# Kernel tuning notes

Measured on AMD Instinct MI355X. Metric: run time of the kernel, lower is better.

## Reference

```python
import math
import jax, jax.numpy as jnp
import numpy as np

NUM_HEADS = 12
NUM_LANDMARKS = 32

def iterative_inv(mat, n_iter=6):
    # mat: [B, H, m, m] row-stochastic kernel; Newton-Schulz pseudo-inverse
    m = mat.shape[-1]
    I = jnp.eye(m, dtype=mat.dtype)
    K = mat
    # 'else' branch: per-(B,H) normalization by max column sum
    denom = jnp.max(jnp.sum(K, axis=-2), axis=-1)[..., None, None]
    V = jnp.swapaxes(K, -1, -2) / denom
    for _ in range(n_iter):
        KV = jnp.matmul(K, V)
        V = jnp.matmul(0.25 * V, 13.0 * I - jnp.matmul(KV, 15.0 * I - jnp.matmul(KV, 7.0 * I - KV)))
    return V

def setup_inputs() -> dict:
    key = jax.random.key(0)
    k1, k2, k3 = jax.random.split(key, 3)
    B, N, C = 8, 2048, 768
    x = jax.random.normal(k1, (B, N, C), dtype=jnp.float32)
    w_qkv = jax.random.normal(k2, (C, 3 * C), dtype=jnp.float32) * (1.0 / math.sqrt(C))
    w_proj = jax.random.normal(k3, (C, C), dtype=jnp.float32) * (1.0 / math.sqrt(C))
    b_proj = jnp.zeros((C,), dtype=jnp.float32)
    return {"x": x, "w_qkv": w_qkv, "w_proj": w_proj, "b_proj": b_proj}

def reference(x, w_qkv, w_proj, b_proj):
    B, N, C = x.shape
    H = NUM_HEADS
    d = C // H
    m = NUM_LANDMARKS
    qkv = (x @ w_qkv).reshape(B, N, 3, H, d).transpose(2, 0, 3, 1, 4)  # [3,B,H,N,d]
    Q, K, V = qkv[0], qkv[1], qkv[2]
    scale = 1.0 / math.sqrt(math.sqrt(d))
    Q = Q * scale
    K = K * scale
    # landmark pooling: mean over contiguous chunks of size N//m
    Q_l = Q.reshape(B, H, m, N // m, d).mean(axis=-2)  # [B,H,m,d]
    K_l = K.reshape(B, H, m, N // m, d).mean(axis=-2)
    kernel_1 = jax.nn.softmax(jnp.einsum('bhnd,bhmd->bhnm', Q, K_l), axis=-1)   # [B,H,N,m]
    kernel_2 = jax.nn.softmax(jnp.einsum('bhmd,bhkd->bhmk', Q_l, K_l), axis=-1) # [B,H,m,m]
    kernel_3 = jax.nn.softmax(jnp.einsum('bhmd,bhnd->bhmn', Q_l, K), axis=-1)   # [B,H,m,N]
    X = jnp.matmul(jnp.matmul(kernel_1, iterative_inv(kernel_2)), jnp.matmul(kernel_3, V))  # [B,H,N,d]
    X = X.transpose(0, 2, 1, 3).reshape(B, N, C)
    return X @ w_proj + b_proj
```

## Files before the change

### kernel.cpp

```cpp
#include <hip/hip_runtime.h>
#include <hip/hip_bf16.h>

typedef __hip_bfloat16 bf16;
typedef __attribute__((ext_vector_type(8))) __bf16 bf16x8;
typedef __attribute__((ext_vector_type(4))) float f32x4;

#define NB 8
#define SEQ 2048
#define CH 768
#define NH 12
#define HD 64
#define NL 32
#define BHT (NB*NH)
#define TOK (NB*SEQ)
#define QK_SCALE 0.35355339059327379f

#define BAR() __builtin_amdgcn_s_barrier()
#define WLGKM0() __asm__ __volatile__("s_waitcnt lgkmcnt(0)" ::: "memory")
#define WVM(n) __asm__ __volatile__("s_waitcnt vmcnt(" #n ")" ::: "memory")

__device__ __forceinline__ void async_ld16(const bf16* g, bf16* l) {
    unsigned loff = (unsigned)__builtin_amdgcn_readfirstlane((int)(unsigned)(uintptr_t)l);
    __builtin_amdgcn_global_load_lds(
        (const __attribute__((address_space(1))) unsigned*)(uintptr_t)g,
        (__attribute__((address_space(3))) unsigned*)(uintptr_t)loff, 16, 0, 0);
}

__global__ void convert_x(const float* __restrict__ x, bf16* __restrict__ xb) {
    size_t i = ((size_t)blockIdx.x * 256 + threadIdx.x) * 8;
    float4 a = *reinterpret_cast<const float4*>(x + i);
    float4 b = *reinterpret_cast<const float4*>(x + i + 4);
    alignas(16) bf16 tmp[8];
    tmp[0] = __float2bfloat16(a.x); tmp[1] = __float2bfloat16(a.y);
    tmp[2] = __float2bfloat16(a.z); tmp[3] = __float2bfloat16(a.w);
    tmp[4] = __float2bfloat16(b.x); tmp[5] = __float2bfloat16(b.y);
    tmp[6] = __float2bfloat16(b.z); tmp[7] = __float2bfloat16(b.w);
    *reinterpret_cast<uint4*>(xb + i) = *reinterpret_cast<const uint4*>(tmp);
}

__global__ void transpose_f32(const float* __restrict__ in, bf16* __restrict__ outp,
                              int Hrows, int Wcols) {
    __shared__ float tile[32][33];
    int bx = blockIdx.x * 32, by = blockIdx.y * 32;
    int tx = threadIdx.x, ty = threadIdx.y;
    for (int i = 0; i < 32; i += 8)
        tile[ty + i][tx] = in[(size_t)(by + ty + i) * Wcols + bx + tx];
    __syncthreads();
    for (int i = 0; i < 32; i += 8)
        outp[(size_t)(bx + ty + i) * Hrows + by + tx] = __float2bfloat16(tile[tx][ty + i]);
}

template <int EPI>
__global__ __launch_bounds__(512, 2) void gemm_bt(
    const bf16* __restrict__ A, const bf16* __restrict__ Bt,
    int Nout, int Kdim,
    bf16* __restrict__ q, bf16* __restrict__ k, bf16* __restrict__ vt,
    float* __restrict__ Ql, float* __restrict__ Kl,
    float* __restrict__ outp, const float* __restrict__ bias_f) {
    __shared__ __align__(16) bf16 As[2][256 * 64];
    __shared__ __align__(16) bf16 Bs[2][192 * 64];
    const int t = threadIdx.x;
    const int wave = t >> 6, lane = t & 63;
    const int quad = lane >> 4, l15 = lane & 15;
    const int wr = wave >> 2, wc = wave & 3;

    int p = blockIdx.y * gridDim.x + blockIdx.x;
    int xcd = p & 7, j = p >> 3;
    int gx = gridDim.x;
    int bn = j % gx;
    int bm = (j / gx) * 8 + xcd;
    const int bm0 = bm * 256;
    const int bn0 = bn * 192;

    const int T = Kdim >> 6;

    const int srow = t >> 3;
    const int scol = (((t & 7) ^ (srow & 7)) << 3);
    const bf16* Abase = A + (size_t)(bm0 + srow) * Kdim + scol;
    const bf16* Bbase = Bt + (size_t)(bn0 + srow) * Kdim + scol;

    auto stA = [&](int kt, int c) {
        async_ld16(Abase + (size_t)(c * 64) * Kdim + kt * 64,
                   &As[kt & 1][c * 4096 + t * 8]);
    };
    auto stB = [&](int kt, int c) {
        async_ld16(Bbase + (size_t)(c * 64) * Kdim + kt * 64,
                   &Bs[kt & 1][c * 4096 + t * 8]);
    };

    const int swk[2] = { (quad ^ (l15 & 7)) << 3, ((4 + quad) ^ (l15 & 7)) << 3 };
    const bf16* arow = &As[0][(wr * 128 + l15) * 64];
    const bf16* brow = &Bs[0][(wc * 48 + l15) * 64];

    f32x4 acc[8][3];
    const f32x4 zero4 = {0.f, 0.f, 0.f, 0.f};
    #pragma unroll
    for (int i = 0; i < 8; i++)
        #pragma unroll
        for (int jj = 0; jj < 3; jj++) acc[i][jj] = zero4;

    stA(0, 0); stA(0, 2); stB(0, 0); stB(0, 1); stB(0, 2); stA(0, 1); stA(0, 3);
    WVM(2);
    BAR();

    bf16x8 a[4][2], b[3][2];
    #pragma unroll 2
    for (int kt = 0; kt < T; kt++) {
        const int cur = kt & 1;
        const bool nxt = (kt + 1 < T);
        const bf16* ab = arow + cur * 16384;
        const bf16* bb = brow + cur * 12288;

        #pragma unroll
        for (int mi = 0; mi < 4; mi++)
            #pragma unroll
            for (int kk = 0; kk < 2; kk++)
                a[mi][kk] = *reinterpret_cast<const bf16x8*>(ab + mi * 1024 + swk[kk]);
        #pragma unroll
        for (int ni = 0; ni < 2; ni++)
            #pragma unroll
            for (int kk = 0; kk < 2; kk++)
                b[ni][kk] = *reinterpret_cast<const bf16x8*>(bb + ni * 1024 + swk[kk]);
        if (nxt) { stA(kt + 1, 0); stA(kt + 1, 2); }
        BAR(); WLGKM0();
        __builtin_amdgcn_s_setprio(1);
        #pragma unroll
        for (int mi = 0; mi < 4; mi++)
            #pragma unroll
            for (int ni = 0; ni < 2; ni++)
                #pragma unroll
                for (int kk = 0; kk < 2; kk++)
                    acc[mi][ni] = __builtin_amdgcn_mfma_f32_16x16x32_bf16(a[mi][kk], b[ni][kk], acc[mi][ni], 0, 0, 0);
        __builtin_amdgcn_s_setprio(0);
        BAR();

        #pragma unroll
        for (int kk = 0; kk < 2; kk++)
            b[2][kk] = *reinterpret_cast<const bf16x8*>(bb + 2 * 1024 + swk[kk]);
        if (nxt) { stB(kt + 1, 0); stB(kt + 1, 1); }
        BAR(); WLGKM0();
        __builtin_amdgcn_s_setprio(1);
        #pragma unroll
        for (int mi = 0; mi < 4; mi++)
            #pragma unroll
            for (int kk = 0; kk < 2; kk++)
                acc[mi][2] = __builtin_amdgcn_mfma_f32_16x16x32_bf16(a[mi][kk], b[2][kk], acc[mi][2], 0, 0, 0);
        __builtin_amdgcn_s_setprio(0);
        if (nxt) { WVM(4); } else { WVM(0); }
        BAR();

        #pragma unroll
        for (int mi = 0; mi < 4; mi++)
            #pragma unroll
            for (int kk = 0; kk < 2; kk++)
                a[mi][kk] = *reinterpret_cast<const bf16x8*>(ab + (mi + 4) * 1024 + swk[kk]);
        if (nxt) { stB(kt + 1, 2); stA(kt + 1, 1); }
        BAR(); WLGKM0();
        __builtin_amdgcn_s_setprio(1);
        #pragma unroll
        for (int mi = 0; mi < 4; mi++)
            #pragma unroll
            for (int ni = 0; ni < 2; ni++)
                #pragma unroll
                for (int kk = 0; kk < 2; kk++)
                    acc[mi + 4][ni] = __builtin_amdgcn_mfma_f32_16x16x32_bf16(a[mi][kk], b[ni][kk], acc[mi + 4][ni], 0, 0, 0);
        __builtin_amdgcn_s_setprio(0);
        BAR();

        if (nxt) { stA(kt + 1, 3); }
        BAR();
        __builtin_amdgcn_s_setprio(1);
        #pragma unroll
        for (int mi = 0; mi < 4; mi++)
            #pragma unroll
            for (int kk = 0; kk < 2; kk++)
                acc[mi + 4][2] = __builtin_amdgcn_mfma_f32_16x16x32_bf16(a[mi][kk], b[2][kk], acc[mi + 4][2], 0, 0, 0);
        __builtin_amdgcn_s_setprio(0);
        WVM(2);
        BAR();
    }

    if (EPI == 0) {
        const int which = bn0 / CH;
        const int rem0 = bn0 - which * CH + wc * 48;
        const int b = bm0 >> 11;
        const int nnb = (bm0 & 2047) + wr * 128;
        if (which < 2) {
            bf16* dstqk = (which == 0) ? q : k;
            float* dstl = (which == 0) ? Ql : Kl;
            const int la0 = nnb >> 6;
            #pragma unroll
            for (int hf = 0; hf < 2; hf++) {
                #pragma unroll
                for (int ni = 0; ni < 3; ni++) {
                    int rem = rem0 + ni * 16;
                    int h = rem >> 6;
                    int dd = (rem & 63) + l15;
                    int bh = b * NH + h;
                    float colsum = 0.f;
                    #pragma unroll
                    for (int m2 = 0; m2 < 4; m2++) {
                        int mi = hf * 4 + m2;
                        int nn0 = nnb + mi * 16 + quad * 4;
                        #pragma unroll
                        for (int r = 0; r < 4; r++) {
                            float val = acc[mi][ni][r];
                            colsum += val;
                            dstqk[((size_t)bh * SEQ + nn0 + r) * HD + dd] = __float2bfloat16(val * QK_SCALE);
                        }
                    }
                    colsum += __shfl_xor(colsum, 16);
                    colsum += __shfl_xor(colsum, 32);
                    if (quad == 0)
                        dstl[((size_t)bh * NL + la0 + hf) * HD + dd] = colsum * (QK_SCALE / 64.f);
                }
            }
        } else {
            #pragma unroll
            for (int ni = 0; ni < 3; ni++) {
                int rem = rem0 + ni * 16;
                int h = rem >> 6;
                int dd = (rem & 63) + l15;
                int bh = b * NH + h;
                #pragma unroll
                for (int mi = 0; mi < 8; mi++) {
                    int nn0 = nnb + mi * 16 + quad * 4;
                    alignas(8) bf16 four[4];
                    #pragma unroll
                    for (int r = 0; r < 4; r++) four[r] = __float2bfloat16(acc[mi][ni][r]);
                    *reinterpret_cast<uint2*>(&vt[((size_t)bh * HD + dd) * SEQ + nn0]) =
                        *reinterpret_cast<const uint2*>(four);
                }
            }
        }
    } else {
        #pragma unroll
        for (int ni = 0; ni < 3; ni++) {
            int col = bn0 + wc * 48 + ni * 16 + l15;
            float bb = bias_f[col];
            #pragma unroll
            for (int mi = 0; mi < 8; mi++)
                #pragma unroll
                for (int r = 0; r < 4; r++) {
                    int row = bm0 + wr * 128 + mi * 16 + quad * 4 + r;
                    outp[(size_t)row * Nout + col] = acc[mi][ni][r] + bb;
                }
        }
    }
}

__device__ inline void mm32(float* Cm, const float* Am, const float* Bm, int t) {
    for (int e = t; e < 1024; e += 256) {
        int i = e >> 5, jj = e & 31;
        float s = 0.f;
        #pragma unroll
        for (int kk = 0; kk < 32; kk++) s += Am[i * 32 + kk] * Bm[kk * 32 + jj];
        Cm[e] = s;
    }
}

__global__ __launch_bounds__(256) void k3_pv(const float* __restrict__ Ql,
                                             const float* __restrict__ Klm,
                                             const bf16* __restrict__ Kb,
                                             const bf16* __restrict__ Vt,
                                             float* __restrict__ Opart,
                                             float* __restrict__ Spart,
                                             float* __restrict__ Vinv) {
    __shared__ __align__(16) char smem[69632];
    const int bh = blockIdx.x;
    const int t = threadIdx.x;

    if (blockIdx.y == 0) {
        float* K2 = (float*)smem;
        float* Vv = K2 + 1024;
        float* KV = K2 + 2048;
        float* Ta = K2 + 3072;
        float* Tb = K2 + 4096;
        float* red = K2 + 5120;
        const float* ql = Ql + (size_t)bh * NL * HD;
        const float* kl = Klm + (size_t)bh * NL * HD;

        for (int e = t; e < 1024; e += 256) {
            int i = e >> 5, jj = e & 31;
            float s = 0.f;
            #pragma unroll 8
            for (int d = 0; d < 64; d++) s += ql[i * 64 + d] * kl[jj * 64 + d];
            K2[e] = s;
        }
        __syncthreads();
        if (t < 32) {
            float mx = -1e30f;
            for (int jj = 0; jj < 32; jj++) mx = fmaxf(mx, K2[t * 32 + jj]);
            float sm = 0.f;
            for (int jj = 0; jj < 32; jj++) { float e = __expf(K2[t * 32 + jj] - mx); K2[t * 32 + jj] = e; sm += e; }
            float inv = 1.f / sm;
            for (int jj = 0; jj < 32; jj++) K2[t * 32 + jj] *= inv;
        }
        __syncthreads();
        if (t < 32) {
            float cs = 0.f;
            for (int i = 0; i < 32; i++) cs += K2[i * 32 + t];
            red[t] = cs;
        }
        __syncthreads();
        if (t == 0) {
            float mx = red[0];
            for (int jj = 1; jj < 32; jj++) mx = fmaxf(mx, red[jj]);
            red[32] = mx;
        }
        __syncthreads();
        float invden = 1.f / red[32];
        for (int e = t; e < 1024; e += 256) {
            int i = e >> 5, jj = e & 31;
            Vv[e] = K2[jj * 32 + i] * invden;
        }
        __syncthreads();
        for (int it = 0; it < 6; it++) {
            mm32(KV, K2, Vv, t);
            __syncthreads();
            for (int e = t; e < 1024; e += 256) { int i = e >> 5, jj = e & 31; Ta[e] = ((i == jj) ? 7.f : 0.f) - KV[e]; }
            __syncthreads();
            mm32(Tb, KV, Ta, t);
            __syncthreads();
            for (int e = t; e < 1024; e += 256) { int i = e >> 5, jj = e & 31; Tb[e] = ((i == jj) ? 15.f : 0.f) - Tb[e]; }
            __syncthreads();
            mm32(Ta, KV, Tb, t);
            __syncthreads();
            for (int e = t; e < 1024; e += 256) { int i = e >> 5, jj = e & 31; Ta[e] = ((i == jj) ? 13.f : 0.f) - Ta[e]; }
            __syncthreads();
            mm32(Tb, Vv, Ta, t);
            __syncthreads();
            for (int e = t; e < 1024; e += 256) Vv[e] = 0.25f * Tb[e];
            __syncthreads();
        }
        for (int e = t; e < 1024; e += 256)
            Vinv[(size_t)bh * 1024 + e] = Vv[e];
        return;
    }

    bf16* Pw0 = (bf16*)smem;
    float* Ored0 = (float*)(smem + 34816);
    float* Sred = (float*)(smem + 34816 + 33280);
    const int cc = blockIdx.y - 1;
    const int n0 = cc * 512;
    const int w = t >> 6, lane = t & 63;
    const int quad = lane >> 4, l15 = lane & 15;

    const bf16* Kbh = Kb + (size_t)bh * SEQ * HD;
    const bf16* Vtb = Vt + (size_t)bh * HD * SEQ;

    bf16x8 af[2][2];
    #pragma unroll
    for (int mt = 0; mt < 2; mt++)
        #pragma unroll
        for (int kh = 0; kh < 2; kh++) {
            const float* src = Ql + (size_t)bh * NL * HD + (mt * 16 + l15) * 64 + kh * 32 + quad * 8;
            alignas(16) bf16 tmp[8];
            #pragma unroll
            for (int jj = 0; jj < 8; jj++) tmp[jj] = __float2bfloat16(src[jj]);
            af[mt][kh] = *reinterpret_cast<const bf16x8*>(tmp);
        }

    const f32x4 zero4 = {0.f, 0.f, 0.f, 0.f};
    f32x4 oacc[2][4];
    #pragma unroll
    for (int mt = 0; mt < 2; mt++)
        #pragma unroll
        for (int nd = 0; nd < 4; nd++) oacc[mt][nd] = zero4;
    float rs[2][4];
    #pragma unroll
    for (int mt = 0; mt < 2; mt++)
        #pragma unroll
        for (int r = 0; r < 4; r++) rs[mt][r] = 0.f;

    bf16* Pme = Pw0 + w * (32 * 136);

    #pragma unroll
    for (int h = 0; h < 2; h++) {
        f32x4 sacc[2][4];
        #pragma unroll
        for (int mt = 0; mt < 2; mt++)
            #pragma unroll
            for (int nt = 0; nt < 4; nt++) sacc[mt][nt] = zero4;
        #pragma unroll
        for (int nt = 0; nt < 4; nt++) {
            int n = n0 + w * 128 + h * 64 + nt * 16 + l15;
            bf16x8 kf0 = *reinterpret_cast<const bf16x8*>(&Kbh[(size_t)n * HD + quad * 8]);
            bf16x8 kf1 = *reinterpret_cast<const bf16x8*>(&Kbh[(size_t)n * HD + 32 + quad * 8]);
            #pragma unroll
            for (int mt = 0; mt < 2; mt++) {
                sacc[mt][nt] = __builtin_amdgcn_mfma_f32_16x16x32_bf16(af[mt][0], kf0, sacc[mt][nt], 0, 0, 0);
                sacc[mt][nt] = __builtin_amdgcn_mfma_f32_16x16x32_bf16(af[mt][1], kf1, sacc[mt][nt], 0, 0, 0);
            }
        }
        #pragma unroll
        for (int mt = 0; mt < 2; mt++)
            #pragma unroll
            for (int nt = 0; nt < 4; nt++)
                #pragma unroll
                for (int r = 0; r < 4; r++) {
                    float pv = __expf(sacc[mt][nt][r]);
                    rs[mt][r] += pv;
                    int row = mt * 16 + quad * 4 + r;
                    Pme[row * 136 + h * 64 + nt * 16 + l15] = __float2bfloat16(pv);
                }
    }
    __asm__ __volatile__("s_waitcnt lgkmcnt(0)" ::: "memory");

    #pragma unroll
    for (int kt = 0; kt < 4; kt++) {
        bf16x8 pa[2];
        pa[0] = *reinterpret_cast<const bf16x8*>(&Pme[l15 * 136 + kt * 32 + quad * 8]);
        pa[1] = *reinterpret_cast<const bf16x8*>(&Pme[(16 + l15) * 136 + kt * 32 + quad * 8]);
        int kbase = n0 + w * 128 + kt * 32 + quad * 8;
        #pragma unroll
        for (int nd = 0; nd < 4; nd++) {
            bf16x8 bv = *reinterpret_cast<const bf16x8*>(&Vtb[(size_t)(nd * 16 + l15) * SEQ + kbase]);
            oacc[0][nd] = __builtin_amdgcn_mfma_f32_16x16x32_bf16(pa[0], bv, oacc[0][nd], 0, 0, 0);
            oacc[1][nd] = __builtin_amdgcn_mfma_f32_16x16x32_bf16(pa[1], bv, oacc[1][nd], 0, 0, 0);
        }
    }

    #pragma unroll
    for (int mt = 0; mt < 2; mt++)
        #pragma unroll
        for (int r = 0; r < 4; r++) {
            float v = rs[mt][r];
            #pragma unroll
            for (int o = 1; o < 16; o <<= 1) v += __shfl_xor(v, o);
            rs[mt][r] = v;
        }
    if (l15 == 0)
        #pragma unroll
        for (int mt = 0; mt < 2; mt++)
            #pragma unroll
            for (int r = 0; r < 4; r++)
                Sred[w * 32 + mt * 16 + quad * 4 + r] = rs[mt][r];
    #pragma unroll
    for (int mt = 0; mt < 2; mt++)
        #pragma unroll
        for (int nd = 0; nd < 4; nd++)
            #pragma unroll
            for (int r = 0; r < 4; r++)
                Ored0[w * (32 * 65) + (mt * 16 + quad * 4 + r) * 65 + nd * 16 + l15] = oacc[mt][nd][r];
    __syncthreads();

    float* Op = Opart + ((size_t)bh * 4 + cc) * (NL * HD);
    for (int e = t; e < 2048; e += 256) {
        int m = e >> 6, dd = e & 63;
        Op[e] = Ored0[0 * (32 * 65) + m * 65 + dd] + Ored0[1 * (32 * 65) + m * 65 + dd] +
                Ored0[2 * (32 * 65) + m * 65 + dd] + Ored0[3 * (32 * 65) + m * 65 + dd];
    }
    if (t < 32)
        Spart[((size_t)bh * 4 + cc) * NL + t] = Sred[t] + Sred[32 + t] + Sred[64 + t] + Sred[96 + t];
}

__global__ __launch_bounds__(256) void combine_w2(const float* __restrict__ Opart,
                                                  const float* __restrict__ Spart,
                                                  const float* __restrict__ Vinv,
                                                  float* __restrict__ W2) {
    __shared__ float K3[2048];
    __shared__ float Vv[1024];
    __shared__ float stot[32];
    const int bh = blockIdx.x;
    const int t = threadIdx.x;

    if (t < 32) {
        const float* sp = Spart + (size_t)bh * 4 * NL;
        stot[t] = sp[t] + sp[32 + t] + sp[64 + t] + sp[96 + t];
    }
    {
        const float* op = Opart + (size_t)bh * 4 * (NL * HD);
        for (int e = t; e < 2048; e += 256)
            K3[e] = op[e] + op[2048 + e] + op[4096 + e] + op[6144 + e];
    }
    for (int e = t; e < 1024; e += 256)
        Vv[e] = Vinv[(size_t)bh * 1024 + e];
    __syncthreads();
    for (int e = t; e < 2048; e += 256) K3[e] *= (1.f / stot[e >> 6]);
    __syncthreads();
    for (int e = t; e < 2048; e += 256) {
        int i = e >> 6, dd = e & 63;
        float s = 0.f;
        #pragma unroll
        for (int kk = 0; kk < 32; kk++) s += Vv[i * 32 + kk] * K3[kk * 64 + dd];
        W2[(size_t)bh * NL * HD + e] = s;
    }
}

__global__ __launch_bounds__(256) void rows_fused(const bf16* __restrict__ Qb,
                                                  const float* __restrict__ Kl,
                                                  const float* __restrict__ W2,
                                                  bf16* __restrict__ Xp) {
    __shared__ __align__(16) bf16 Klb[32 * 64];
    __shared__ __align__(16) bf16 W2t[64 * 32];
    __shared__ __align__(16) bf16 Pw[4][32 * 40];
    const int bh = blockIdx.x, tile = blockIdx.y;
    const int t = threadIdx.x, w = t >> 6, lane = t & 63;
    const int quad = lane >> 4, l15 = lane & 15;

    {
        const float* ksrc = Kl + (size_t)bh * NL * HD;
        const float* wsrc = W2 + (size_t)bh * NL * HD;
        int e0 = t * 8;
        #pragma unroll
        for (int jj = 0; jj < 8; jj++) {
            int e = e0 + jj;
            Klb[e] = __float2bfloat16(ksrc[e]);
            int kk = e >> 6, dd = e & 63;
            W2t[dd * 32 + kk] = __float2bfloat16(wsrc[e]);
        }
    }
    __syncthreads();

    const int b = bh / NH, h = bh - b * NH;
    const int row0 = tile * 128 + w * 32;
    const bf16* qbase = Qb + ((size_t)bh * SEQ + row0) * HD;

    const f32x4 zero4 = {0.f, 0.f, 0.f, 0.f};
    f32x4 sacc[2][2];
    #pragma unroll
    for (int mt = 0; mt < 2; mt++)
        #pragma unroll
        for (int nt = 0; nt < 2; nt++) sacc[mt][nt] = zero4;
    #pragma unroll
    for (int kh = 0; kh < 2; kh++) {
        bf16x8 bk0 = *reinterpret_cast<const bf16x8*>(&Klb[(l15) * 64 + kh * 32 + quad * 8]);
        bf16x8 bk1 = *reinterpret_cast<const bf16x8*>(&Klb[(16 + l15) * 64 + kh * 32 + quad * 8]);
        #pragma unroll
        for (int mt = 0; mt < 2; mt++) {
            bf16x8 aq = *reinterpret_cast<const bf16x8*>(&qbase[(size_t)(mt * 16 + l15) * HD + kh * 32 + quad * 8]);
            sacc[mt][0] = __builtin_amdgcn_mfma_f32_16x16x32_bf16(aq, bk0, sacc[mt][0], 0, 0, 0);
            sacc[mt][1] = __builtin_amdgcn_mfma_f32_16x16x32_bf16(aq, bk1, sacc[mt][1], 0, 0, 0);
        }
    }

    float invs[2][4];
    bf16* Pme = &Pw[w][0];
    #pragma unroll
    for (int mt = 0; mt < 2; mt++)
        #pragma unroll
        for (int r = 0; r < 4; r++) {
            float v0 = __expf(sacc[mt][0][r]);
            float v1 = __expf(sacc[mt][1][r]);
            int row = mt * 16 + quad * 4 + r;
            Pme[row * 40 + l15] = __float2bfloat16(v0);
            Pme[row * 40 + 16 + l15] = __float2bfloat16(v1);
            float v = v0 + v1;
            #pragma unroll
            for (int o = 1; o < 16; o <<= 1) v += __shfl_xor(v, o);
            invs[mt][r] = 1.f / v;
        }
    __asm__ __volatile__("s_waitcnt lgkmcnt(0)" ::: "memory");

    f32x4 oacc[2][4];
    #pragma unroll
    for (int mt = 0; mt < 2; mt++)
        #pragma unroll
        for (int nd = 0; nd < 4; nd++) oacc[mt][nd] = zero4;
    bf16x8 pa[2];
    pa[0] = *reinterpret_cast<const bf16x8*>(&Pme[l15 * 40 + quad * 8]);
    pa[1] = *reinterpret_cast<const bf16x8*>(&Pme[(16 + l15) * 40 + quad * 8]);
    #pragma unroll
    for (int nd = 0; nd < 4; nd++) {
        bf16x8 bw = *reinterpret_cast<const bf16x8*>(&W2t[(nd * 16 + l15) * 32 + quad * 8]);
        oacc[0][nd] = __builtin_amdgcn_mfma_f32_16x16x32_bf16(pa[0], bw, oacc[0][nd], 0, 0, 0);
        oacc[1][nd] = __builtin_amdgcn_mfma_f32_16x16x32_bf16(pa[1], bw, oacc[1][nd], 0, 0, 0);
    }

    #pragma unroll
    for (int mt = 0; mt < 2; mt++)
        #pragma unroll
        for (int nd = 0; nd < 4; nd++)
            #pragma unroll
            for (int r = 0; r < 4; r++) {
                int row = row0 + mt * 16 + quad * 4 + r;
                Xp[((size_t)(b * SEQ + row)) * CH + h * 64 + nd * 16 + l15] =
                    __float2bfloat16(oacc[mt][nd][r] * invs[mt][r]);
            }
}

extern "C" void kernel_launch(void* const* d_in, const int* in_sizes, int n_in,
                              void* d_out, int out_size, void* d_ws, size_t ws_size,
                              hipStream_t stream) {
    const float* x      = (const float*)d_in[0];
    const float* w_qkv  = (const float*)d_in[1];
    const float* w_proj = (const float*)d_in[2];
    const float* b_proj = (const float*)d_in[3];
    float* out = (float*)d_out;

    char* ws = (char*)d_ws;
    size_t off = 0;
    auto alloc = [&](size_t bytes) -> void* {
        void* p = ws + off;
        off += (bytes + 255) & ~(size_t)255;
        return p;
    };
    bf16* wqkvT  = (bf16*)alloc((size_t)3 * CH * CH * 2);
    bf16* wprojT = (bf16*)alloc((size_t)CH * CH * 2);
    bf16* Qb     = (bf16*)alloc((size_t)BHT * SEQ * HD * 2);
    bf16* Kb     = (bf16*)alloc((size_t)BHT * SEQ * HD * 2);
    bf16* Vt     = (bf16*)alloc((size_t)BHT * SEQ * HD * 2);
    float* Ql    = (float*)alloc((size_t)BHT * NL * HD * 4);
    float* Kl    = (float*)alloc((size_t)BHT * NL * HD * 4);
    float* Opart = (float*)alloc((size_t)BHT * 4 * NL * HD * 4);
    float* Spart = (float*)alloc((size_t)BHT * 4 * NL * 4);
    float* Vinv  = (float*)alloc((size_t)BHT * NL * NL * 4);
    float* W2    = (float*)alloc((size_t)BHT * NL * HD * 4);
    bf16* Xp     = (bf16*)alloc((size_t)TOK * CH * 2);
    if (ws_size < off) return;
    bf16* xb = Xp;

    convert_x<<<TOK * CH / 2048, 256, 0, stream>>>(x, xb);
    transpose_f32<<<dim3((3 * CH) / 32, CH / 32), dim3(32, 8), 0, stream>>>(w_qkv, wqkvT, CH, 3 * CH);
    transpose_f32<<<dim3(CH / 32, CH / 32), dim3(32, 8), 0, stream>>>(w_proj, wprojT, CH, CH);

    gemm_bt<0><<<dim3((3 * CH) / 192, TOK / 256), 512, 0, stream>>>(
        xb, wqkvT, 3 * CH, CH, Qb, Kb, Vt, Ql, Kl, nullptr, nullptr);

    k3_pv<<<dim3(BHT, 5), 256, 0, stream>>>(Ql, Kl, Kb, Vt, Opart, Spart, Vinv);
    combine_w2<<<BHT, 256, 0, stream>>>(Opart, Spart, Vinv, W2);
    rows_fused<<<dim3(BHT, SEQ / 128), 256, 0, stream>>>(Qb, Kl, W2, Xp);

    gemm_bt<1><<<dim3(CH / 192, TOK / 256), 512, 0, stream>>>(
        Xp, wprojT, CH, CH, nullptr, nullptr, nullptr, nullptr, nullptr, out, b_proj);
}
```

Before: 277.2 us.

## Fuse prep kernels, merge landmark inverse with PV pass, remap GEMM tiles

Merges the x conversion and both weight transposes into one prep launch. Fuses the Newton-Schulz inverse, the kernel_3·V pass and the W2 combine into a single kernel per (batch, head), removing the Opart/Spart/Vinv round trips and two launches. The price is that each block now runs the inverse and then loops serially over all 2048 tokens, so parallelism drops from 480 blocks to 96. Also changes the GEMM tile mapping so each XCD gets a contiguous range of row tiles.

```diff
diff --git a/kernel.cpp b/kernel.cpp
--- a/kernel.cpp
+++ b/kernel.cpp
@@ -26,23 +26,38 @@
         (__attribute__((address_space(3))) unsigned*)(uintptr_t)loff, 16, 0, 0);
 }
 
-__global__ void convert_x(const float* __restrict__ x, bf16* __restrict__ xb) {
-    size_t i = ((size_t)blockIdx.x * 256 + threadIdx.x) * 8;
-    float4 a = *reinterpret_cast<const float4*>(x + i);
-    float4 b = *reinterpret_cast<const float4*>(x + i + 4);
-    alignas(16) bf16 tmp[8];
-    tmp[0] = __float2bfloat16(a.x); tmp[1] = __float2bfloat16(a.y);
-    tmp[2] = __float2bfloat16(a.z); tmp[3] = __float2bfloat16(a.w);
-    tmp[4] = __float2bfloat16(b.x); tmp[5] = __float2bfloat16(b.y);
-    tmp[6] = __float2bfloat16(b.z); tmp[7] = __float2bfloat16(b.w);
-    *reinterpret_cast<uint4*>(xb + i) = *reinterpret_cast<const uint4*>(tmp);
-}
-
-__global__ void transpose_f32(const float* __restrict__ in, bf16* __restrict__ outp,
-                              int Hrows, int Wcols) {
+#define PREP_G0 (TOK*CH/2048)
+#define PREP_G1 ((3*CH/32)*(CH/32))
+#define PREP_G2 ((CH/32)*(CH/32))
+__global__ __launch_bounds__(256) void prep(const float* __restrict__ x, bf16* __restrict__ xb,
+                                            const float* __restrict__ w_qkv, bf16* __restrict__ wqkvT,
+                                            const float* __restrict__ w_proj, bf16* __restrict__ wprojT) {
     __shared__ float tile[32][33];
-    int bx = blockIdx.x * 32, by = blockIdx.y * 32;
-    int tx = threadIdx.x, ty = threadIdx.y;
+    const int bid = blockIdx.x;
+    const int t = threadIdx.x;
+    if (bid < PREP_G0) {
+        size_t i = ((size_t)bid * 256 + t) * 8;
+        float4 a = *reinterpret_cast<const float4*>(x + i);
+        float4 b = *reinterpret_cast<const float4*>(x + i + 4);
+        alignas(16) bf16 tmp[8];
+        tmp[0] = __float2bfloat16(a.x); tmp[1] = __float2bfloat16(a.y);
+        tmp[2] = __float2bfloat16(a.z); tmp[3] = __float2bfloat16(a.w);
+        tmp[4] = __float2bfloat16(b.x); tmp[5] = __float2bfloat16(b.y);
+        tmp[6] = __float2bfloat16(b.z); tmp[7] = __float2bfloat16(b.w);
+        *reinterpret_cast<uint4*>(xb + i) = *reinterpret_cast<const uint4*>(tmp);
+        return;
+    }
+    const float* in; bf16* outp; int Hrows, Wcols, bx, by;
+    if (bid < PREP_G0 + PREP_G1) {
+        int tb = bid - PREP_G0;
+        in = w_qkv; outp = wqkvT; Hrows = CH; Wcols = 3 * CH;
+        bx = (tb % (3 * CH / 32)) * 32; by = (tb / (3 * CH / 32)) * 32;
+    } else {
+        int tb = bid - PREP_G0 - PREP_G1;
+        in = w_proj; outp = wprojT; Hrows = CH; Wcols = CH;
+        bx = (tb % (CH / 32)) * 32; by = (tb / (CH / 32)) * 32;
+    }
+    int tx = t & 31, ty = t >> 5;
     for (int i = 0; i < 32; i += 8)
         tile[ty + i][tx] = in[(size_t)(by + ty + i) * Wcols + bx + tx];
     __syncthreads();
@@ -65,10 +80,10 @@
     const int wr = wave >> 2, wc = wave & 3;
 
     int p = blockIdx.y * gridDim.x + blockIdx.x;
-    int xcd = p & 7, j = p >> 3;
+    int xcd = p & 7, g = p >> 3;
     int gx = gridDim.x;
-    int bn = j % gx;
-    int bm = (j / gx) * 8 + xcd;
+    int bn = g % gx;
+    int bm = xcd * (gridDim.y >> 3) + g / gx;
     const int bm0 = bm * 256;
     const int bn0 = bn * 192;
 
@@ -259,93 +274,85 @@
     }
 }
 
-__global__ __launch_bounds__(256) void k3_pv(const float* __restrict__ Ql,
-                                             const float* __restrict__ Klm,
-                                             const bf16* __restrict__ Kb,
-                                             const bf16* __restrict__ Vt,
-                                             float* __restrict__ Opart,
-                                             float* __restrict__ Spart,
-                                             float* __restrict__ Vinv) {
-    __shared__ __align__(16) char smem[69632];
+__global__ __launch_bounds__(256) void k3w2(const float* __restrict__ Ql,
+                                            const float* __restrict__ Klm,
+                                            const bf16* __restrict__ Kb,
+                                            const bf16* __restrict__ Vt,
+                                            float* __restrict__ W2) {
+    __shared__ __align__(16) char smem[72704];
+    float* Vv  = (float*)smem;
+    float* K2  = (float*)(smem + 4096);
+    float* KV  = (float*)(smem + 8192);
+    float* Ta  = (float*)(smem + 12288);
+    float* Tb  = (float*)(smem + 16384);
+    float* red = (float*)(smem + 20480);
+    bf16*  Pw0 = (bf16*)(smem + 4096);
+    float* Ored0 = (float*)(smem + 38912);
+    float* Sred  = (float*)(smem + 72192);
+    float* K3    = (float*)(smem + 4096);
+    float* stot  = (float*)(smem + 12288);
+
     const int bh = blockIdx.x;
     const int t = threadIdx.x;
-
-    if (blockIdx.y == 0) {
-        float* K2 = (float*)smem;
-        float* Vv = K2 + 1024;
-        float* KV = K2 + 2048;
-        float* Ta = K2 + 3072;
-        float* Tb = K2 + 4096;
-        float* red = K2 + 5120;
-        const float* ql = Ql + (size_t)bh * NL * HD;
-        const float* kl = Klm + (size_t)bh * NL * HD;
-
-        for (int e = t; e < 1024; e += 256) {
-            int i = e >> 5, jj = e & 31;
-            float s = 0.f;
-            #pragma unroll 8
-            for (int d = 0; d < 64; d++) s += ql[i * 64 + d] * kl[jj * 64 + d];
-            K2[e] = s;
-        }
-        __syncthreads();
-        if (t < 32) {
-            float mx = -1e30f;
-            for (int jj = 0; jj < 32; jj++) mx = fmaxf(mx, K2[t * 32 + jj]);
-            float sm = 0.f;
-            for (int jj = 0; jj < 32; jj++) { float e = __expf(K2[t * 32 + jj] - mx); K2[t * 32 + jj] = e; sm += e; }
-            float inv = 1.f / sm;
-            for (int jj = 0; jj < 32; jj++) K2[t * 32 + jj] *= inv;
-        }
-        __syncthreads();
-        if (t < 32) {
-            float cs = 0.f;
-            for (int i = 0; i < 32; i++) cs += K2[i * 32 + t];
-            red[t] = cs;
-        }
-        __syncthreads();
-        if (t == 0) {
-            float mx = red[0];
-            for (int jj = 1; jj < 32; jj++) mx = fmaxf(mx, red[jj]);
-            red[32] = mx;
-        }
-        __syncthreads();
-        float invden = 1.f / red[32];
-        for (int e = t; e < 1024; e += 256) {
-            int i = e >> 5, jj = e & 31;
-            Vv[e] = K2[jj * 32 + i] * invden;
-        }
-        __syncthreads();
-        for (int it = 0; it < 6; it++) {
-            mm32(KV, K2, Vv, t);
-            __syncthreads();
-            for (int e = t; e < 1024; e += 256) { int i = e >> 5, jj = e & 31; Ta[e] = ((i == jj) ? 7.f : 0.f) - KV[e]; }
-            __syncthreads();
-            mm32(Tb, KV, Ta, t);
-            __syncthreads();
-            for (int e = t; e < 1024; e += 256) { int i = e >> 5, jj = e & 31; Tb[e] = ((i == jj) ? 15.f : 0.f) - Tb[e]; }
-            __syncthreads();
-            mm32(Ta, KV, Tb, t);
-            __syncthreads();
-            for (int e = t; e < 1024; e += 256) { int i = e >> 5, jj = e & 31; Ta[e] = ((i == jj) ? 13.f : 0.f) - Ta[e]; }
-            __syncthreads();
-            mm32(Tb, Vv, Ta, t);
-            __syncthreads();
-            for (int e = t; e < 1024; e += 256) Vv[e] = 0.25f * Tb[e];
-            __syncthreads();
-        }
-        for (int e = t; e < 1024; e += 256)
-            Vinv[(size_t)bh * 1024 + e] = Vv[e];
-        return;
-    }
-
-    bf16* Pw0 = (bf16*)smem;
-    float* Ored0 = (float*)(smem + 34816);
-    float* Sred = (float*)(smem + 34816 + 33280);
-    const int cc = blockIdx.y - 1;
-    const int n0 = cc * 512;
+    const float* ql = Ql + (size_t)bh * NL * HD;
+    const float* kl = Klm + (size_t)bh * NL * HD;
+
+    for (int e = t; e < 1024; e += 256) {
+        int i = e >> 5, jj = e & 31;
+        float s = 0.f;
+        #pragma unroll 8
+        for (int d = 0; d < 64; d++) s += ql[i * 64 + d] * kl[jj * 64 + d];
+        K2[e] = s;
+    }
+    __syncthreads();
+    if (t < 32) {
+        float mx = -1e30f;
+        for (int jj = 0; jj < 32; jj++) mx = fmaxf(mx, K2[t * 32 + jj]);
+        float sm = 0.f;
+        for (int jj = 0; jj < 32; jj++) { float e = __expf(K2[t * 32 + jj] - mx); K2[t * 32 + jj] = e; sm += e; }
+        float inv = 1.f / sm;
+        for (int jj = 0; jj < 32; jj++) K2[t * 32 + jj] *= inv;
+    }
+    __syncthreads();
+    if (t < 32) {
+        float cs = 0.f;
+        for (int i = 0; i < 32; i++) cs += K2[i * 32 + t];
+        red[t] = cs;
+    }
+    __syncthreads();
+    if (t == 0) {
+        float mx = red[0];
+        for (int jj = 1; jj < 32; jj++) mx = fmaxf(mx, red[jj]);
+        red[32] = mx;
+    }
+    __syncthreads();
+    float invden = 1.f / red[32];
+    for (int e = t; e < 1024; e += 256) {
+        int i = e >> 5, jj = e & 31;
+        Vv[e] = K2[jj * 32 + i] * invden;
+    }
+    __syncthreads();
+    for (int it = 0; it < 6; it++) {
+        mm32(KV, K2, Vv, t);
+        __syncthreads();
+        for (int e = t; e < 1024; e += 256) { int i = e >> 5, jj = e & 31; Ta[e] = ((i == jj) ? 7.f : 0.f) - KV[e]; }
+        __syncthreads();
+        mm32(Tb, KV, Ta, t);
+        __syncthreads();
+        for (int e = t; e < 1024; e += 256) { int i = e >> 5, jj = e & 31; Tb[e] = ((i == jj) ? 15.f : 0.f) - Tb[e]; }
+        __syncthreads();
+        mm32(Ta, KV, Tb, t);
+        __syncthreads();
+        for (int e = t; e < 1024; e += 256) { int i = e >> 5, jj = e & 31; Ta[e] = ((i == jj) ? 13.f : 0.f) - Ta[e]; }
+        __syncthreads();
+        mm32(Tb, Vv, Ta, t);
+        __syncthreads();
+        for (int e = t; e < 1024; e += 256) Vv[e] = 0.25f * Tb[e];
+        __syncthreads();
+    }
+
     const int w = t >> 6, lane = t & 63;
     const int quad = lane >> 4, l15 = lane & 15;
-
     const bf16* Kbh = Kb + (size_t)bh * SEQ * HD;
     const bf16* Vtb = Vt + (size_t)bh * HD * SEQ;
 
@@ -354,7 +361,7 @@
     for (int mt = 0; mt < 2; mt++)
         #pragma unroll
         for (int kh = 0; kh < 2; kh++) {
-            const float* src = Ql + (size_t)bh * NL * HD + (mt * 16 + l15) * 64 + kh * 32 + quad * 8;
+            const float* src = ql + (mt * 16 + l15) * 64 + kh * 32 + quad * 8;
             alignas(16) bf16 tmp[8];
             #pragma unroll
             for (int jj = 0; jj < 8; jj++) tmp[jj] = __float2bfloat16(src[jj]);
@@ -375,49 +382,52 @@
 
     bf16* Pme = Pw0 + w * (32 * 136);
 
-    #pragma unroll
-    for (int h = 0; h < 2; h++) {
-        f32x4 sacc[2][4];
-        #pragma unroll
-        for (int mt = 0; mt < 2; mt++)
-            #pragma unroll
-            for (int nt = 0; nt < 4; nt++) sacc[mt][nt] = zero4;
-        #pragma unroll
-        for (int nt = 0; nt < 4; nt++) {
-            int n = n0 + w * 128 + h * 64 + nt * 16 + l15;
-            bf16x8 kf0 = *reinterpret_cast<const bf16x8*>(&Kbh[(size_t)n * HD + quad * 8]);
-            bf16x8 kf1 = *reinterpret_cast<const bf16x8*>(&Kbh[(size_t)n * HD + 32 + quad * 8]);
-            #pragma unroll
-            for (int mt = 0; mt < 2; mt++) {
-                sacc[mt][nt] = __builtin_amdgcn_mfma_f32_16x16x32_bf16(af[mt][0], kf0, sacc[mt][nt], 0, 0, 0);
-                sacc[mt][nt] = __builtin_amdgcn_mfma_f32_16x16x32_bf16(af[mt][1], kf1, sacc[mt][nt], 0, 0, 0);
+    for (int cc = 0; cc < 4; cc++) {
+        const int base = cc * 512 + w * 128;
+        #pragma unroll
+        for (int h = 0; h < 2; h++) {
+            f32x4 sacc[2][4];
+            #pragma unroll
+            for (int mt = 0; mt < 2; mt++)
+                #pragma unroll
+                for (int nt = 0; nt < 4; nt++) sacc[mt][nt] = zero4;
+            #pragma unroll
+            for (int nt = 0; nt < 4; nt++) {
+                int n = base + h * 64 + nt * 16 + l15;
+                bf16x8 kf0 = *reinterpret_cast<const bf16x8*>(&Kbh[(size_t)n * HD + quad * 8]);
+                bf16x8 kf1 = *reinterpret_cast<const bf16x8*>(&Kbh[(size_t)n * HD + 32 + quad * 8]);
+                #pragma unroll
+                for (int mt = 0; mt < 2; mt++) {
+                    sacc[mt][nt] = __builtin_amdgcn_mfma_f32_16x16x32_bf16(af[mt][0], kf0, sacc[mt][nt], 0, 0, 0);
+                    sacc[mt][nt] = __builtin_amdgcn_mfma_f32_16x16x32_bf16(af[mt][1], kf1, sacc[mt][nt], 0, 0, 0);
+                }
             }
-        }
-        #pragma unroll
-        for (int mt = 0; mt < 2; mt++)
-            #pragma unroll
-            for (int nt = 0; nt < 4; nt++)
-                #pragma unroll
-                for (int r = 0; r < 4; r++) {
-                    float pv = __expf(sacc[mt][nt][r]);
-                    rs[mt][r] += pv;
-                    int row = mt * 16 + quad * 4 + r;
-                    Pme[row * 136 + h * 64 + nt * 16 + l15] = __float2bfloat16(pv);
-                }
-    }
-    __asm__ __volatile__("s_waitcnt lgkmcnt(0)" ::: "memory");
-
-    #pragma unroll
-    for (int kt = 0; kt < 4; kt++) {
-        bf16x8 pa[2];
-        pa[0] = *reinterpret_cast<const bf16x8*>(&Pme[l15 * 136 + kt * 32 + quad * 8]);
-        pa[1] = *reinterpret_cast<const bf16x8*>(&Pme[(16 + l15) * 136 + kt * 32 + quad * 8]);
-        int kbase = n0 + w * 128 + kt * 32 + quad * 8;
-        #pragma unroll
-        for (int nd = 0; nd < 4; nd++) {
-            bf16x8 bv = *reinterpret_cast<const bf16x8*>(&Vtb[(size_t)(nd * 16 + l15) * SEQ + kbase]);
-            oacc[0][nd] = __builtin_amdgcn_mfma_f32_16x16x32_bf16(pa[0], bv, oacc[0][nd], 0, 0, 0);
-            oacc[1][nd] = __builtin_amdgcn_mfma_f32_16x16x32_bf16(pa[1], bv, oacc[1][nd], 0, 0, 0);
+            #pragma unroll
+            for (int mt = 0; mt < 2; mt++)
+                #pragma unroll
+                for (int nt = 0; nt < 4; nt++)
+                    #pragma unroll
+                    for (int r = 0; r < 4; r++) {
+                        float pv = __expf(sacc[mt][nt][r]);
+                        rs[mt][r] += pv;
+                        int row = mt * 16 + quad * 4 + r;
+                        Pme[row * 136 + h * 64 + nt * 16 + l15] = __float2bfloat16(pv);
+                    }
+        }
+        __asm__ __volatile__("s_waitcnt lgkmcnt(0)" ::: "memory");
+
+        #pragma unroll
+        for (int kt = 0; kt < 4; kt++) {
+            bf16x8 pa[2];
+            pa[0] = *reinterpret_cast<const bf16x8*>(&Pme[l15 * 136 + kt * 32 + quad * 8]);
+            pa[1] = *reinterpret_cast<const bf16x8*>(&Pme[(16 + l15) * 136 + kt * 32 + quad * 8]);
+            int kbase = base + kt * 32 + quad * 8;
+            #pragma unroll
+            for (int nd = 0; nd < 4; nd++) {
+                bf16x8 bv = *reinterpret_cast<const bf16x8*>(&Vtb[(size_t)(nd * 16 + l15) * SEQ + kbase]);
+                oacc[0][nd] = __builtin_amdgcn_mfma_f32_16x16x32_bf16(pa[0], bv, oacc[0][nd], 0, 0, 0);
+                oacc[1][nd] = __builtin_amdgcn_mfma_f32_16x16x32_bf16(pa[1], bv, oacc[1][nd], 0, 0, 0);
+            }
         }
     }
 
@@ -445,40 +455,17 @@
                 Ored0[w * (32 * 65) + (mt * 16 + quad * 4 + r) * 65 + nd * 16 + l15] = oacc[mt][nd][r];
     __syncthreads();
 
-    float* Op = Opart + ((size_t)bh * 4 + cc) * (NL * HD);
+    if (t < 32)
+        stot[t] = Sred[t] + Sred[32 + t] + Sred[64 + t] + Sred[96 + t];
+    __syncthreads();
     for (int e = t; e < 2048; e += 256) {
         int m = e >> 6, dd = e & 63;
-        Op[e] = Ored0[0 * (32 * 65) + m * 65 + dd] + Ored0[1 * (32 * 65) + m * 65 + dd] +
-                Ored0[2 * (32 * 65) + m * 65 + dd] + Ored0[3 * (32 * 65) + m * 65 + dd];
-    }
-    if (t < 32)
-        Spart[((size_t)bh * 4 + cc) * NL + t] = Sred[t] + Sred[32 + t] + Sred[64 + t] + Sred[96 + t];
-}
-
-__global__ __launch_bounds__(256) void combine_w2(const float* __restrict__ Opart,
-                                                  const float* __restrict__ Spart,
-                                                  const float* __restrict__ Vinv,
-                                                  float* __restrict__ W2) {
-    __shared__ float K3[2048];
-    __shared__ float Vv[1024];
-    __shared__ float stot[32];
-    const int bh = blockIdx.x;
-    const int t = threadIdx.x;
-
-    if (t < 32) {
-        const float* sp = Spart + (size_t)bh * 4 * NL;
-        stot[t] = sp[t] + sp[32 + t] + sp[64 + t] + sp[96 + t];
-    }
-    {
-        const float* op = Opart + (size_t)bh * 4 * (NL * HD);
-        for (int e = t; e < 2048; e += 256)
-            K3[e] = op[e] + op[2048 + e] + op[4096 + e] + op[6144 + e];
-    }
-    for (int e = t; e < 1024; e += 256)
-        Vv[e] = Vinv[(size_t)bh * 1024 + e];
-    __syncthreads();
-    for (int e = t; e < 2048; e += 256) K3[e] *= (1.f / stot[e >> 6]);
-    __syncthreads();
+        float s = Ored0[0 * (32 * 65) + m * 65 + dd] + Ored0[1 * (32 * 65) + m * 65 + dd] +
+                  Ored0[2 * (32 * 65) + m * 65 + dd] + Ored0[3 * (32 * 65) + m * 65 + dd];
+        K3[e] = s * (1.f / stot[m]);
+    }
+    __syncthreads();
+
     for (int e = t; e < 2048; e += 256) {
         int i = e >> 6, dd = e & 63;
         float s = 0.f;
@@ -603,23 +590,17 @@
     bf16* Vt     = (bf16*)alloc((size_t)BHT * SEQ * HD * 2);
     float* Ql    = (float*)alloc((size_t)BHT * NL * HD * 4);
     float* Kl    = (float*)alloc((size_t)BHT * NL * HD * 4);
-    float* Opart = (float*)alloc((size_t)BHT * 4 * NL * HD * 4);
-    float* Spart = (float*)alloc((size_t)BHT * 4 * NL * 4);
-    float* Vinv  = (float*)alloc((size_t)BHT * NL * NL * 4);
     float* W2    = (float*)alloc((size_t)BHT * NL * HD * 4);
     bf16* Xp     = (bf16*)alloc((size_t)TOK * CH * 2);
     if (ws_size < off) return;
     bf16* xb = Xp;
 
-    convert_x<<<TOK * CH / 2048, 256, 0, stream>>>(x, xb);
-    transpose_f32<<<dim3((3 * CH) / 32, CH / 32), dim3(32, 8), 0, stream>>>(w_qkv, wqkvT, CH, 3 * CH);
-    transpose_f32<<<dim3(CH / 32, CH / 32), dim3(32, 8), 0, stream>>>(w_proj, wprojT, CH, CH);
+    prep<<<PREP_G0 + PREP_G1 + PREP_G2, 256, 0, stream>>>(x, xb, w_qkv, wqkvT, w_proj, wprojT);
 
     gemm_bt<0><<<dim3((3 * CH) / 192, TOK / 256), 512, 0, stream>>>(
         xb, wqkvT, 3 * CH, CH, Qb, Kb, Vt, Ql, Kl, nullptr, nullptr);
 
-    k3_pv<<<dim3(BHT, 5), 256, 0, stream>>>(Ql, Kl, Kb, Vt, Opart, Spart, Vinv);
-    combine_w2<<<BHT, 256, 0, stream>>>(Opart, Spart, Vinv, W2);
+    k3w2<<<BHT, 256, 0, stream>>>(Ql, Kl, Kb, Vt, W2);
     rows_fused<<<dim3(BHT, SEQ / 128), 256, 0, stream>>>(Qb, Kl, W2, Xp);
 
     gemm_bt<1><<<dim3(CH / 192, TOK / 256), 512, 0, stream>>>(
```

Measured after the change: 292.8 us. 1.06x slower.
